# Optimization experiments

Measured on AMD Instinct MI355X. Metric: run time of the kernel, lower is better.

The kernel has to match this reference:

```python
import jax, jax.numpy as jnp
import numpy as np

N = 100000   # nodes
C = 128      # in_channels
K = 32       # n_super_nodes
B = 64       # graphs (num segments)


def setup_inputs() -> dict:
    key = jax.random.key(0)
    k_x, k_b, k_w1, k_b1, k_w2, k_b2 = jax.random.split(key, 6)
    x = jax.random.normal(k_x, (N, C), dtype=jnp.float32)
    batch = jnp.sort(jax.random.randint(k_b, (N,), 0, B))
    # assign_mlp params: Linear(C,C) -> ReLU -> Linear(C,K); stored as [in,out]
    W1 = jax.random.normal(k_w1, (C, C), dtype=jnp.float32) / np.sqrt(C)
    b1 = jax.random.normal(k_b1, (C,), dtype=jnp.float32) * 0.01
    W2 = jax.random.normal(k_w2, (C, K), dtype=jnp.float32) / np.sqrt(C)
    b2 = jax.random.normal(k_b2, (K,), dtype=jnp.float32) * 0.01
    return {"x": x, "batch": batch, "W1": W1, "b1": b1, "W2": W2, "b2": b2}


def reference(x, batch, W1, b1, W2, b2):
    # assignment logits: MLP over node features
    h = jax.nn.relu(x @ W1 + b1)          # [N, C]
    s = jax.nn.softmax(h @ W2 + b2, axis=-1)  # [N, K]
    # outer product per node, then scatter-sum by graph id
    x_expanded = x[:, None, :] * s[:, :, None]  # [N, K, C]
    out = jax.ops.segment_sum(x_expanded, batch, num_segments=B)  # [B, K, C]
    return (out, s)
```

## Files before the change

kernel.cpp:

```cpp
#include <hip/hip_runtime.h>
#include <hip/hip_bf16.h>

#define NN 100000
#define CC 128
#define KK 32
#define BB 64
#define CH 2
#define NCHUNK (NN / 32)

typedef __bf16 bf16x8 __attribute__((ext_vector_type(8)));
typedef float  f32x4  __attribute__((ext_vector_type(4)));

__device__ __forceinline__ unsigned short f2bf(float v) {
    union { __bf16 h; unsigned short s; } u;
    u.h = (__bf16)v;
    return u.s;
}
__device__ __forceinline__ float bf2f(unsigned short h) {
    union { unsigned u; float f; } a; a.u = ((unsigned)h) << 16;
    return a.f;
}
__device__ __forceinline__ void unpack_hilo(uint4 a, uint4 b,
                                            bf16x8& hi8, bf16x8& lo8) {
    union { unsigned u[4]; bf16x8 v; } H, L;
    H.u[0] = __builtin_amdgcn_perm(a.y, a.x, 0x05040100u);
    H.u[1] = __builtin_amdgcn_perm(a.w, a.z, 0x05040100u);
    H.u[2] = __builtin_amdgcn_perm(b.y, b.x, 0x05040100u);
    H.u[3] = __builtin_amdgcn_perm(b.w, b.z, 0x05040100u);
    L.u[0] = __builtin_amdgcn_perm(a.y, a.x, 0x07060302u);
    L.u[1] = __builtin_amdgcn_perm(a.w, a.z, 0x07060302u);
    L.u[2] = __builtin_amdgcn_perm(b.y, b.x, 0x07060302u);
    L.u[3] = __builtin_amdgcn_perm(b.w, b.z, 0x07060302u);
    hi8 = H.v; lo8 = L.v;
}

__device__ __forceinline__ void atomAddF(float* p, float v) {
#if defined(__gfx950__) || defined(__gfx942__) || defined(__gfx90a__)
    unsafeAtomicAdd(p, v);
#else
    atomicAdd(p, v);
#endif
}

__global__ __launch_bounds__(256) void hp_prep(const float* __restrict__ W1,
                                               const float* __restrict__ W2,
                                               unsigned short* __restrict__ w1f,
                                               unsigned short* __restrict__ w2f,
                                               float* __restrict__ out_zero) {
    const int t = blockIdx.x * 256 + threadIdx.x;
    {
        const int idx  = t;
        const int j    = idx & 7;
        const int lane = (idx >> 3) & 63;
        const int nt   = (idx >> 9) & 7;
        const int kt   = idx >> 12;
        const int k = kt * 32 + (lane >> 4) * 8 + j;
        const int n = nt * 16 + (lane & 15);
        const float w = W1[k * CC + n];
        const unsigned short h = f2bf(w);
        w1f[idx]         = h;
        w1f[16384 + idx] = f2bf(w - bf2f(h));
    }
    if (t < 4096) {
        const int idx  = t;
        const int j    = idx & 7;
        const int lane = (idx >> 3) & 63;
        const int nt   = (idx >> 9) & 1;
        const int kt   = idx >> 10;
        const int k = kt * 32 + (lane >> 4) * 8 + j;
        const int n = nt * 16 + (lane & 15);
        const float w = W2[k * KK + n];
        const unsigned short h = f2bf(w);
        w2f[idx]        = h;
        w2f[4096 + idx] = f2bf(w - bf2f(h));
    }
    const float4 z = make_float4(0.f, 0.f, 0.f, 0.f);
    for (int i = t; i < BB * KK * CC / 4; i += 16384)
        *(float4*)(out_zero + (size_t)i * 4) = z;
}

__global__ __launch_bounds__(256, 3) void hp_fused(
    const float* __restrict__ x,
    const unsigned short* __restrict__ w1f,
    const unsigned short* __restrict__ w2f,
    const float* __restrict__ b1,
    const float* __restrict__ b2,
    const int* __restrict__ batch,
    float* __restrict__ s_out,
    float* __restrict__ out)
{
    __shared__ __align__(16) char uni[16896];
    __shared__ __align__(16) unsigned short xbL[8 * 64 * 8];
    __shared__ float lgT[32][36];

    unsigned short* xa   = (unsigned short*)uni;
    unsigned int*   hs16 = (unsigned int*)uni;

    const int t    = threadIdx.x;
    const int wave = __builtin_amdgcn_readfirstlane(t >> 6);
    const int lane = t & 63;

    const int pmt   = wave & 1;
    const int chalf = wave >> 1;
    const int nrow  = (lane >> 4) * 8;

    const float b2lo = b2[lane & 15];
    const float b2hi = b2[16 + (lane & 15)];

    f32x4 pacc[4];
    #pragma unroll
    for (int i = 0; i < 4; ++i) pacc[i] = (f32x4){0.f, 0.f, 0.f, 0.f};

    int cg = __builtin_amdgcn_readfirstlane(batch[blockIdx.x * (CH * 32)]);

    auto flush = [&](int g) {
        float* op = out + (size_t)g * KK * CC;
        #pragma unroll
        for (int i = 0; i < 4; ++i) {
            const int c = (chalf * 4 + i) * 16 + (lane & 15);
            #pragma unroll
            for (int r = 0; r < 4; ++r) {
                const int k = pmt * 16 + (lane >> 4) * 4 + r;
                atomAddF(op + k * CC + c, pacc[i][r]);
            }
            pacc[i] = (f32x4){0.f, 0.f, 0.f, 0.f};
        }
    };

    #pragma unroll 1
    for (int ch = 0; ch < CH; ++ch) {
        const int chunk = blockIdx.x * CH + ch;
        if (chunk >= NCHUNK) break;
        const int base = chunk * 32;

        __syncthreads();

        #pragma unroll
        for (int mt = 0; mt < 2; ++mt) {
            const int q  = mt * 4 + wave;
            const int n  = base + mt * 16 + (lane & 15);
            const int ck = wave * 32 + (lane >> 4) * 8;
            const float4 va = *(const float4*)(x + (size_t)n * CC + ck);
            const float4 vb = *(const float4*)(x + (size_t)n * CC + ck + 4);
            const float v[8] = {va.x, va.y, va.z, va.w, vb.x, vb.y, vb.z, vb.w};
            union { unsigned short s[8]; uint4 u; } H, L;
            #pragma unroll
            for (int j = 0; j < 8; ++j) {
                H.s[j] = f2bf(v[j]);
                L.s[j] = f2bf(v[j] - bf2f(H.s[j]));
            }
            unsigned short* d0 = xa + (q * 64 + lane) * 8;
            *(uint4*)(d0)        = H.u;
            *(uint4*)(d0 + 4096) = L.u;
        }

        #pragma unroll
        for (int cc = 0; cc < 2; ++cc) {
            const int ct = wave * 2 + cc;
            const int c  = ct * 16 + (lane & 15);
            const int nb = base + nrow;
            union { unsigned short s[8]; uint4 u; } Hb;
            #pragma unroll
            for (int j = 0; j < 8; ++j)
                Hb.s[j] = f2bf(x[(size_t)(nb + j) * CC + c]);
            *(uint4*)(xbL + ((size_t)ct * 64 + lane) * 8) = Hb.u;
        }
        __syncthreads();

        f32x4 acc[2][2];
        #pragma unroll
        for (int mt = 0; mt < 2; ++mt)
            #pragma unroll
            for (int nl = 0; nl < 2; ++nl)
                acc[mt][nl] = (f32x4){0.f, 0.f, 0.f, 0.f};

        #pragma unroll
        for (int kt = 0; kt < 4; ++kt) {
            bf16x8 ah[2], al[2];
            #pragma unroll
            for (int mt = 0; mt < 2; ++mt) {
                ah[mt] = *(const bf16x8*)(xa + ((mt * 4 + kt) * 64 + lane) * 8);
                al[mt] = *(const bf16x8*)(xa + 4096 + ((mt * 4 + kt) * 64 + lane) * 8);
            }
            #pragma unroll
            for (int nl = 0; nl < 2; ++nl) {
                const int nt = 2 * wave + nl;
                const bf16x8 wh = *(const bf16x8*)(w1f + ((kt * 8 + nt) * 64 + lane) * 8);
                const bf16x8 wl = *(const bf16x8*)(w1f + 16384 + ((kt * 8 + nt) * 64 + lane) * 8);
                #pragma unroll
                for (int mt = 0; mt < 2; ++mt) {
                    acc[mt][nl] = __builtin_amdgcn_mfma_f32_16x16x32_bf16(ah[mt], wh, acc[mt][nl], 0, 0, 0);
                    acc[mt][nl] = __builtin_amdgcn_mfma_f32_16x16x32_bf16(al[mt], wh, acc[mt][nl], 0, 0, 0);
                    acc[mt][nl] = __builtin_amdgcn_mfma_f32_16x16x32_bf16(ah[mt], wl, acc[mt][nl], 0, 0, 0);
                }
            }
        }
        __syncthreads();

        #pragma unroll
        for (int nl = 0; nl < 2; ++nl) {
            const int c = (2 * wave + nl) * 16 + (lane & 15);
            const float bv = b1[c];
            #pragma unroll
            for (int mt = 0; mt < 2; ++mt)
                #pragma unroll
                for (int r = 0; r < 4; ++r) {
                    const int node = mt * 16 + (lane >> 4) * 4 + r;
                    const float h = fmaxf(acc[mt][nl][r] + bv, 0.f);
                    const unsigned short hi = f2bf(h);
                    const unsigned short lo = f2bf(h - bf2f(hi));
                    hs16[node * 132 + c] = (unsigned)hi | ((unsigned)lo << 16);
                }
        }
        __syncthreads();

        if (wave < 2) {
            const int mt2 = wave;
            f32x4 dacc[2];
            dacc[0] = (f32x4){0.f, 0.f, 0.f, 0.f};
            dacc[1] = (f32x4){0.f, 0.f, 0.f, 0.f};
            #pragma unroll
            for (int kt = 0; kt < 4; ++kt) {
                const unsigned* hp = hs16 + (mt2 * 16 + (lane & 15)) * 132
                                          + kt * 32 + (lane >> 4) * 8;
                const uint4 u0 = *(const uint4*)hp;
                const uint4 u1 = *(const uint4*)(hp + 4);
                bf16x8 ah, al;
                unpack_hilo(u0, u1, ah, al);
                #pragma unroll
                for (int nt2 = 0; nt2 < 2; ++nt2) {
                    const bf16x8 wh = *(const bf16x8*)(w2f + ((kt * 2 + nt2) * 64 + lane) * 8);
                    const bf16x8 wl = *(const bf16x8*)(w2f + 4096 + ((kt * 2 + nt2) * 64 + lane) * 8);
                    dacc[nt2] = __builtin_amdgcn_mfma_f32_16x16x32_bf16(ah, wh, dacc[nt2], 0, 0, 0);
                    dacc[nt2] = __builtin_amdgcn_mfma_f32_16x16x32_bf16(al, wh, dacc[nt2], 0, 0, 0);
                    dacc[nt2] = __builtin_amdgcn_mfma_f32_16x16x32_bf16(ah, wl, dacc[nt2], 0, 0, 0);
                }
            }
            float lg0[4], lg1[4], m[4];
            #pragma unroll
            for (int r = 0; r < 4; ++r) {
                lg0[r] = dacc[0][r] + b2lo;
                lg1[r] = dacc[1][r] + b2hi;
                m[r] = fmaxf(lg0[r], lg1[r]);
            }
            #pragma unroll
            for (int msk = 1; msk < 16; msk <<= 1)
                #pragma unroll
                for (int r = 0; r < 4; ++r)
                    m[r] = fmaxf(m[r], __shfl_xor(m[r], msk));
            float e0[4], e1[4], sm[4];
            #pragma unroll
            for (int r = 0; r < 4; ++r) {
                e0[r] = __expf(lg0[r] - m[r]);
                e1[r] = __expf(lg1[r] - m[r]);
                sm[r] = e0[r] + e1[r];
            }
            #pragma unroll
            for (int msk = 1; msk < 16; msk <<= 1)
                #pragma unroll
                for (int r = 0; r < 4; ++r)
                    sm[r] += __shfl_xor(sm[r], msk);
            #pragma unroll
            for (int r = 0; r < 4; ++r) {
                const float inv = 1.f / sm[r];
                const int node = mt2 * 16 + (lane >> 4) * 4 + r;
                lgT[node][lane & 15]        = e0[r] * inv;
                lgT[node][16 + (lane & 15)] = e1[r] * inv;
            }
        }
        __syncthreads();

        {
            const int node = lane & 31;
            const int koff = ((lane >> 5) << 4) + wave * 4;
            const float4 s4 = *(const float4*)&lgT[node][koff];
            *(float4*)(s_out + (size_t)(base + node) * KK + koff) = s4;
        }

        {
            union { unsigned short s[8]; bf16x8 v; } A;
            const int kA = pmt * 16 + (lane & 15);
            #pragma unroll
            for (int j = 0; j < 8; ++j)
                A.s[j] = f2bf(lgT[nrow + j][kA]);
            bf16x8 Bv[4];
            #pragma unroll
            for (int i = 0; i < 4; ++i)
                Bv[i] = *(const bf16x8*)(xbL + ((size_t)(chalf * 4 + i) * 64 + lane) * 8);

            const int gl0 = __builtin_amdgcn_readfirstlane(batch[base]);
            const int gh  = __builtin_amdgcn_readfirstlane(batch[base + 31]);

            if (gl0 == cg && gh == cg) {
                #pragma unroll
                for (int i = 0; i < 4; ++i)
                    pacc[i] = __builtin_amdgcn_mfma_f32_16x16x32_bf16(A.v, Bv[i], pacc[i], 0, 0, 0);
            } else {
                int bt[8];
                #pragma unroll
                for (int j = 0; j < 8; ++j) bt[j] = batch[base + nrow + j];
                while (cg < gh) {
                    union { unsigned short s[8]; bf16x8 v; } Am;
                    #pragma unroll
                    for (int j = 0; j < 8; ++j)
                        Am.s[j] = (bt[j] == cg) ? A.s[j] : (unsigned short)0;
                    #pragma unroll
                    for (int i = 0; i < 4; ++i)
                        pacc[i] = __builtin_amdgcn_mfma_f32_16x16x32_bf16(Am.v, Bv[i], pacc[i], 0, 0, 0);
                    flush(cg);
                    ++cg;
                }
                union { unsigned short s[8]; bf16x8 v; } Am;
                #pragma unroll
                for (int j = 0; j < 8; ++j)
                    Am.s[j] = (bt[j] == cg) ? A.s[j] : (unsigned short)0;
                #pragma unroll
                for (int i = 0; i < 4; ++i)
                    pacc[i] = __builtin_amdgcn_mfma_f32_16x16x32_bf16(Am.v, Bv[i], pacc[i], 0, 0, 0);
            }
        }
    }

    flush(cg);
}

extern "C" void kernel_launch(void* const* d_in, const int* in_sizes, int n_in,
                              void* d_out, int out_size, void* d_ws, size_t ws_size,
                              hipStream_t stream) {
    const float* x     = (const float*)d_in[0];
    const int*   batch = (const int*)d_in[1];
    const float* W1    = (const float*)d_in[2];
    const float* b1    = (const float*)d_in[3];
    const float* W2    = (const float*)d_in[4];
    const float* b2    = (const float*)d_in[5];

    float* out = (float*)d_out;
    float* s   = out + (size_t)BB * KK * CC;

    char* ws = (char*)d_ws;
    unsigned short* w1f = (unsigned short*)ws;
    unsigned short* w2f = (unsigned short*)(ws + 65536);

    hp_prep<<<64, 256, 0, stream>>>(W1, W2, w1f, w2f, out);
    const int nblk = (NCHUNK + CH - 1) / CH;
    hp_fused<<<nblk, 256, 0, stream>>>(x, w1f, w2f, b1, b2, batch, s, out);
}
```

Measured before the change: 137.2 us.

## Replace output atomics with per-slot partials and prefetch next chunk into registers

Each block now owns twice as many 32-node chunks. While the current chunk is being converted and computed, the block loads the next chunk's x values into registers, and the bf16 x tile buffer is double-buffered in shared memory. The per-graph float atomics on the output are replaced by plain stores into a per-graph, per-slot partial buffer. A slot is derived from segment bounds computed by binary search in the prep kernel. A new reduce kernel sums the 16 slots into the output. This trades atomic contention for an extra launch, a larger workspace to zero and reduce, and more register pressure. It also assumes no graph spans more than 16 blocks.

```diff
diff --git a/kernel.cpp b/kernel.cpp
--- a/kernel.cpp
+++ b/kernel.cpp
@@ -5,8 +5,9 @@
 #define CC 128
 #define KK 32
 #define BB 64
-#define CH 2
+#define CH 4
 #define NCHUNK (NN / 32)
+#define NSLOT 16
 
 typedef __bf16 bf16x8 __attribute__((ext_vector_type(8)));
 typedef float  f32x4  __attribute__((ext_vector_type(4)));
@@ -34,21 +35,24 @@
     hi8 = H.v; lo8 = L.v;
 }
 
-__device__ __forceinline__ void atomAddF(float* p, float v) {
-#if defined(__gfx950__) || defined(__gfx942__) || defined(__gfx90a__)
-    unsafeAtomicAdd(p, v);
-#else
-    atomicAdd(p, v);
-#endif
-}
-
-__global__ __launch_bounds__(256) void hp_prep(const float* __restrict__ W1,
+__global__ __launch_bounds__(256) void hp_prep(const int* __restrict__ batch,
+                                               const float* __restrict__ W1,
                                                const float* __restrict__ W2,
+                                               int* __restrict__ bounds,
                                                unsigned short* __restrict__ w1f,
                                                unsigned short* __restrict__ w2f,
-                                               float* __restrict__ out_zero) {
+                                               float* __restrict__ part) {
+    if (blockIdx.x == 0 && threadIdx.x <= BB) {
+        const int b = threadIdx.x;
+        int lo = 0, hi = NN;
+        while (lo < hi) {
+            const int mid = (lo + hi) >> 1;
+            if (batch[mid] < b) lo = mid + 1; else hi = mid;
+        }
+        bounds[b] = lo;
+    }
     const int t = blockIdx.x * 256 + threadIdx.x;
-    {
+    if (t < 16384) {
         const int idx  = t;
         const int j    = idx & 7;
         const int lane = (idx >> 3) & 63;
@@ -75,8 +79,8 @@
         w2f[4096 + idx] = f2bf(w - bf2f(h));
     }
     const float4 z = make_float4(0.f, 0.f, 0.f, 0.f);
-    for (int i = t; i < BB * KK * CC / 4; i += 16384)
-        *(float4*)(out_zero + (size_t)i * 4) = z;
+    for (int i = t; i < BB * NSLOT * KK * CC / 4; i += 65536)
+        *(float4*)(part + (size_t)i * 4) = z;
 }
 
 __global__ __launch_bounds__(256, 3) void hp_fused(
@@ -86,11 +90,12 @@
     const float* __restrict__ b1,
     const float* __restrict__ b2,
     const int* __restrict__ batch,
+    const int* __restrict__ bounds,
     float* __restrict__ s_out,
-    float* __restrict__ out)
+    float* __restrict__ part)
 {
     __shared__ __align__(16) char uni[16896];
-    __shared__ __align__(16) unsigned short xbL[8 * 64 * 8];
+    __shared__ __align__(16) unsigned short xbL[2][8 * 64 * 8];
     __shared__ float lgT[32][36];
 
     unsigned short* xa   = (unsigned short*)uni;
@@ -104,6 +109,8 @@
     const int chalf = wave >> 1;
     const int nrow  = (lane >> 4) * 8;
 
+    const float bv_epi0 = b1[(2 * wave + 0) * 16 + (lane & 15)];
+    const float bv_epi1 = b1[(2 * wave + 1) * 16 + (lane & 15)];
     const float b2lo = b2[lane & 15];
     const float b2hi = b2[16 + (lane & 15)];
 
@@ -114,18 +121,40 @@
     int cg = __builtin_amdgcn_readfirstlane(batch[blockIdx.x * (CH * 32)]);
 
     auto flush = [&](int g) {
-        float* op = out + (size_t)g * KK * CC;
+        const int slot = blockIdx.x - (bounds[g] >> 7);
+        float* op = part + ((size_t)g * NSLOT + slot) * (KK * CC);
         #pragma unroll
         for (int i = 0; i < 4; ++i) {
             const int c = (chalf * 4 + i) * 16 + (lane & 15);
             #pragma unroll
             for (int r = 0; r < 4; ++r) {
                 const int k = pmt * 16 + (lane >> 4) * 4 + r;
-                atomAddF(op + k * CC + c, pacc[i][r]);
+                op[k * CC + c] = pacc[i][r];
             }
             pacc[i] = (f32x4){0.f, 0.f, 0.f, 0.f};
         }
     };
+
+    float4 pva0, pvb0, pva1, pvb1;
+    float  pxb0[8], pxb1[8];
+    {
+        const int base0 = blockIdx.x * (CH * 32);
+        const int n0 = base0 + (lane & 15);
+        const int n1 = base0 + 16 + (lane & 15);
+        const int ck = wave * 32 + (lane >> 4) * 8;
+        pva0 = *(const float4*)(x + (size_t)n0 * CC + ck);
+        pvb0 = *(const float4*)(x + (size_t)n0 * CC + ck + 4);
+        pva1 = *(const float4*)(x + (size_t)n1 * CC + ck);
+        pvb1 = *(const float4*)(x + (size_t)n1 * CC + ck + 4);
+        const int c0 = (wave * 2 + 0) * 16 + (lane & 15);
+        const int c1 = (wave * 2 + 1) * 16 + (lane & 15);
+        const int nr = base0 + nrow;
+        #pragma unroll
+        for (int j = 0; j < 8; ++j) {
+            pxb0[j] = x[(size_t)(nr + j) * CC + c0];
+            pxb1[j] = x[(size_t)(nr + j) * CC + c1];
+        }
+    }
 
     #pragma unroll 1
     for (int ch = 0; ch < CH; ++ch) {
@@ -133,37 +162,53 @@
         if (chunk >= NCHUNK) break;
         const int base = chunk * 32;
 
-        __syncthreads();
-
-        #pragma unroll
-        for (int mt = 0; mt < 2; ++mt) {
-            const int q  = mt * 4 + wave;
-            const int n  = base + mt * 16 + (lane & 15);
+        {
+            const float v0[8] = {pva0.x, pva0.y, pva0.z, pva0.w,
+                                 pvb0.x, pvb0.y, pvb0.z, pvb0.w};
+            const float v1[8] = {pva1.x, pva1.y, pva1.z, pva1.w,
+                                 pvb1.x, pvb1.y, pvb1.z, pvb1.w};
+            union { unsigned short s[8]; uint4 u; } H0, L0, H1, L1;
+            #pragma unroll
+            for (int j = 0; j < 8; ++j) {
+                H0.s[j] = f2bf(v0[j]); L0.s[j] = f2bf(v0[j] - bf2f(H0.s[j]));
+                H1.s[j] = f2bf(v1[j]); L1.s[j] = f2bf(v1[j] - bf2f(H1.s[j]));
+            }
+            unsigned short* d0 = xa + ((0 * 4 + wave) * 64 + lane) * 8;
+            unsigned short* d1 = xa + ((1 * 4 + wave) * 64 + lane) * 8;
+            *(uint4*)(d0)        = H0.u;
+            *(uint4*)(d0 + 4096) = L0.u;
+            *(uint4*)(d1)        = H1.u;
+            *(uint4*)(d1 + 4096) = L1.u;
+        }
+
+        {
+            union { unsigned short s[8]; uint4 u; } Hb0, Hb1;
+            #pragma unroll
+            for (int j = 0; j < 8; ++j) {
+                Hb0.s[j] = f2bf(pxb0[j]);
+                Hb1.s[j] = f2bf(pxb1[j]);
+            }
+            *(uint4*)(&xbL[ch & 1][((wave * 2 + 0) * 64 + lane) * 8]) = Hb0.u;
+            *(uint4*)(&xbL[ch & 1][((wave * 2 + 1) * 64 + lane) * 8]) = Hb1.u;
+        }
+
+        if (ch + 1 < CH && chunk + 1 < NCHUNK) {
+            const int nb = base + 32;
+            const int n0 = nb + (lane & 15);
+            const int n1 = nb + 16 + (lane & 15);
             const int ck = wave * 32 + (lane >> 4) * 8;
-            const float4 va = *(const float4*)(x + (size_t)n * CC + ck);
-            const float4 vb = *(const float4*)(x + (size_t)n * CC + ck + 4);
-            const float v[8] = {va.x, va.y, va.z, va.w, vb.x, vb.y, vb.z, vb.w};
-            union { unsigned short s[8]; uint4 u; } H, L;
+            pva0 = *(const float4*)(x + (size_t)n0 * CC + ck);
+            pvb0 = *(const float4*)(x + (size_t)n0 * CC + ck + 4);
+            pva1 = *(const float4*)(x + (size_t)n1 * CC + ck);
+            pvb1 = *(const float4*)(x + (size_t)n1 * CC + ck + 4);
+            const int c0 = (wave * 2 + 0) * 16 + (lane & 15);
+            const int c1 = (wave * 2 + 1) * 16 + (lane & 15);
+            const int nr = nb + nrow;
             #pragma unroll
             for (int j = 0; j < 8; ++j) {
-                H.s[j] = f2bf(v[j]);
-                L.s[j] = f2bf(v[j] - bf2f(H.s[j]));
-            }
-            unsigned short* d0 = xa + (q * 64 + lane) * 8;
-            *(uint4*)(d0)        = H.u;
-            *(uint4*)(d0 + 4096) = L.u;
-        }
-
-        #pragma unroll
-        for (int cc = 0; cc < 2; ++cc) {
-            const int ct = wave * 2 + cc;
-            const int c  = ct * 16 + (lane & 15);
-            const int nb = base + nrow;
-            union { unsigned short s[8]; uint4 u; } Hb;
-            #pragma unroll
-            for (int j = 0; j < 8; ++j)
-                Hb.s[j] = f2bf(x[(size_t)(nb + j) * CC + c]);
-            *(uint4*)(xbL + ((size_t)ct * 64 + lane) * 8) = Hb.u;
+                pxb0[j] = x[(size_t)(nr + j) * CC + c0];
+                pxb1[j] = x[(size_t)(nr + j) * CC + c1];
+            }
         }
         __syncthreads();
 
@@ -199,8 +244,8 @@
 
         #pragma unroll
         for (int nl = 0; nl < 2; ++nl) {
+            const float bv = nl ? bv_epi1 : bv_epi0;
             const int c = (2 * wave + nl) * 16 + (lane & 15);
-            const float bv = b1[c];
             #pragma unroll
             for (int mt = 0; mt < 2; ++mt)
                 #pragma unroll
@@ -286,7 +331,7 @@
             bf16x8 Bv[4];
             #pragma unroll
             for (int i = 0; i < 4; ++i)
-                Bv[i] = *(const bf16x8*)(xbL + ((size_t)(chalf * 4 + i) * 64 + lane) * 8);
+                Bv[i] = *(const bf16x8*)(&xbL[ch & 1][((chalf * 4 + i) * 64 + lane) * 8]);
 
             const int gl0 = __builtin_amdgcn_readfirstlane(batch[base]);
             const int gh  = __builtin_amdgcn_readfirstlane(batch[base + 31]);
@@ -324,6 +369,23 @@
     flush(cg);
 }
 
+__global__ __launch_bounds__(256) void hp_reduce(const float* __restrict__ part,
+                                                 float* __restrict__ out) {
+    const int i = (blockIdx.x * 256 + threadIdx.x) * 4;
+    if (i < BB * KK * CC) {
+        const int b = i >> 12;
+        const int j = i & 4095;
+        const float* pp = part + (size_t)b * NSLOT * 4096 + j;
+        float4 r = make_float4(0.f, 0.f, 0.f, 0.f);
+        #pragma unroll 4
+        for (int q = 0; q < NSLOT; ++q) {
+            const float4 v = *(const float4*)(pp + (size_t)q * 4096);
+            r.x += v.x; r.y += v.y; r.z += v.z; r.w += v.w;
+        }
+        *(float4*)(out + i) = r;
+    }
+}
+
 extern "C" void kernel_launch(void* const* d_in, const int* in_sizes, int n_in,
                               void* d_out, int out_size, void* d_ws, size_t ws_size,
                               hipStream_t stream) {
@@ -338,10 +400,13 @@
     float* s   = out + (size_t)BB * KK * CC;
 
     char* ws = (char*)d_ws;
-    unsigned short* w1f = (unsigned short*)ws;
-    unsigned short* w2f = (unsigned short*)(ws + 65536);
-
-    hp_prep<<<64, 256, 0, stream>>>(W1, W2, w1f, w2f, out);
+    int*            bounds = (int*)ws;
+    unsigned short* w1f    = (unsigned short*)(ws + 1024);
+    unsigned short* w2f    = (unsigned short*)(ws + 66560);
+    float*          part   = (float*)(ws + 82944);
+
+    hp_prep<<<256, 256, 0, stream>>>(batch, W1, W2, bounds, w1f, w2f, part);
     const int nblk = (NCHUNK + CH - 1) / CH;
-    hp_fused<<<nblk, 256, 0, stream>>>(x, w1f, w2f, b1, b2, batch, s, out);
-}
+    hp_fused<<<nblk, 256, 0, stream>>>(x, w1f, w2f, b1, b2, batch, bounds, s, part);
+    hp_reduce<<<BB * KK * CC / (256 * 4), 256, 0, stream>>>(part, out);
+}
```

Measured after the change: 173.9 us. +26.7%, slower.

## Replace global atomics with per-block partial slots plus separate reduction kernel

Applied to the files above, without the earlier changes.

Each block now writes its per-graph partial sums to a dedicated slot computed from binary-searched segment bounds, and a new reduce kernel sums 16 slots per graph. This removes contended float atomics on the output. It also doubles chunks per block, double-buffers the xbL tile so one barrier per chunk can be dropped, hoists the b1 bias loads, and moves the s store after the MFMA. In exchange it adds an extra kernel launch, zeroes a much larger partial buffer, and relies on each graph spanning at most 16 blocks (slot = block - bounds>>7).

```diff
diff --git a/kernel.cpp b/kernel.cpp
--- a/kernel.cpp
+++ b/kernel.cpp
@@ -5,8 +5,9 @@
 #define CC 128
 #define KK 32
 #define BB 64
-#define CH 2
+#define CH 4
 #define NCHUNK (NN / 32)
+#define NSLOT 16
 
 typedef __bf16 bf16x8 __attribute__((ext_vector_type(8)));
 typedef float  f32x4  __attribute__((ext_vector_type(4)));
@@ -34,21 +35,24 @@
     hi8 = H.v; lo8 = L.v;
 }
 
-__device__ __forceinline__ void atomAddF(float* p, float v) {
-#if defined(__gfx950__) || defined(__gfx942__) || defined(__gfx90a__)
-    unsafeAtomicAdd(p, v);
-#else
-    atomicAdd(p, v);
-#endif
-}
-
-__global__ __launch_bounds__(256) void hp_prep(const float* __restrict__ W1,
+__global__ __launch_bounds__(256) void hp_prep(const int* __restrict__ batch,
+                                               const float* __restrict__ W1,
                                                const float* __restrict__ W2,
+                                               int* __restrict__ bounds,
                                                unsigned short* __restrict__ w1f,
                                                unsigned short* __restrict__ w2f,
-                                               float* __restrict__ out_zero) {
+                                               float* __restrict__ part) {
+    if (blockIdx.x == 0 && threadIdx.x <= BB) {
+        const int b = threadIdx.x;
+        int lo = 0, hi = NN;
+        while (lo < hi) {
+            const int mid = (lo + hi) >> 1;
+            if (batch[mid] < b) lo = mid + 1; else hi = mid;
+        }
+        bounds[b] = lo;
+    }
     const int t = blockIdx.x * 256 + threadIdx.x;
-    {
+    if (t < 16384) {
         const int idx  = t;
         const int j    = idx & 7;
         const int lane = (idx >> 3) & 63;
@@ -75,8 +79,8 @@
         w2f[4096 + idx] = f2bf(w - bf2f(h));
     }
     const float4 z = make_float4(0.f, 0.f, 0.f, 0.f);
-    for (int i = t; i < BB * KK * CC / 4; i += 16384)
-        *(float4*)(out_zero + (size_t)i * 4) = z;
+    for (int i = t; i < BB * NSLOT * KK * CC / 4; i += 65536)
+        *(float4*)(part + (size_t)i * 4) = z;
 }
 
 __global__ __launch_bounds__(256, 3) void hp_fused(
@@ -86,11 +90,12 @@
     const float* __restrict__ b1,
     const float* __restrict__ b2,
     const int* __restrict__ batch,
+    const int* __restrict__ bounds,
     float* __restrict__ s_out,
-    float* __restrict__ out)
+    float* __restrict__ part)
 {
     __shared__ __align__(16) char uni[16896];
-    __shared__ __align__(16) unsigned short xbL[8 * 64 * 8];
+    __shared__ __align__(16) unsigned short xbL[2][8 * 64 * 8];
     __shared__ float lgT[32][36];
 
     unsigned short* xa   = (unsigned short*)uni;
@@ -104,6 +109,8 @@
     const int chalf = wave >> 1;
     const int nrow  = (lane >> 4) * 8;
 
+    const float bv_epi0 = b1[(2 * wave + 0) * 16 + (lane & 15)];
+    const float bv_epi1 = b1[(2 * wave + 1) * 16 + (lane & 15)];
     const float b2lo = b2[lane & 15];
     const float b2hi = b2[16 + (lane & 15)];
 
@@ -114,14 +121,15 @@
     int cg = __builtin_amdgcn_readfirstlane(batch[blockIdx.x * (CH * 32)]);
 
     auto flush = [&](int g) {
-        float* op = out + (size_t)g * KK * CC;
+        const int slot = blockIdx.x - (bounds[g] >> 7);
+        float* op = part + ((size_t)g * NSLOT + slot) * (KK * CC);
         #pragma unroll
         for (int i = 0; i < 4; ++i) {
             const int c = (chalf * 4 + i) * 16 + (lane & 15);
             #pragma unroll
             for (int r = 0; r < 4; ++r) {
                 const int k = pmt * 16 + (lane >> 4) * 4 + r;
-                atomAddF(op + k * CC + c, pacc[i][r]);
+                op[k * CC + c] = pacc[i][r];
             }
             pacc[i] = (f32x4){0.f, 0.f, 0.f, 0.f};
         }
@@ -132,8 +140,6 @@
         const int chunk = blockIdx.x * CH + ch;
         if (chunk >= NCHUNK) break;
         const int base = chunk * 32;
-
-        __syncthreads();
 
         #pragma unroll
         for (int mt = 0; mt < 2; ++mt) {
@@ -163,7 +169,7 @@
             #pragma unroll
             for (int j = 0; j < 8; ++j)
                 Hb.s[j] = f2bf(x[(size_t)(nb + j) * CC + c]);
-            *(uint4*)(xbL + ((size_t)ct * 64 + lane) * 8) = Hb.u;
+            *(uint4*)(&xbL[ch & 1][((size_t)ct * 64 + lane) * 8]) = Hb.u;
         }
         __syncthreads();
 
@@ -199,8 +205,8 @@
 
         #pragma unroll
         for (int nl = 0; nl < 2; ++nl) {
+            const float bv = nl ? bv_epi1 : bv_epi0;
             const int c = (2 * wave + nl) * 16 + (lane & 15);
-            const float bv = b1[c];
             #pragma unroll
             for (int mt = 0; mt < 2; ++mt)
                 #pragma unroll
@@ -271,13 +277,6 @@
         __syncthreads();
 
         {
-            const int node = lane & 31;
-            const int koff = ((lane >> 5) << 4) + wave * 4;
-            const float4 s4 = *(const float4*)&lgT[node][koff];
-            *(float4*)(s_out + (size_t)(base + node) * KK + koff) = s4;
-        }
-
-        {
             union { unsigned short s[8]; bf16x8 v; } A;
             const int kA = pmt * 16 + (lane & 15);
             #pragma unroll
@@ -286,7 +285,7 @@
             bf16x8 Bv[4];
             #pragma unroll
             for (int i = 0; i < 4; ++i)
-                Bv[i] = *(const bf16x8*)(xbL + ((size_t)(chalf * 4 + i) * 64 + lane) * 8);
+                Bv[i] = *(const bf16x8*)(&xbL[ch & 1][((size_t)(chalf * 4 + i) * 64 + lane) * 8]);
 
             const int gl0 = __builtin_amdgcn_readfirstlane(batch[base]);
             const int gh  = __builtin_amdgcn_readfirstlane(batch[base + 31]);
@@ -319,9 +318,33 @@
                     pacc[i] = __builtin_amdgcn_mfma_f32_16x16x32_bf16(Am.v, Bv[i], pacc[i], 0, 0, 0);
             }
         }
+
+        {
+            const int node = lane & 31;
+            const int koff = ((lane >> 5) << 4) + wave * 4;
+            const float4 s4 = *(const float4*)&lgT[node][koff];
+            *(float4*)(s_out + (size_t)(base + node) * KK + koff) = s4;
+        }
     }
 
     flush(cg);
+}
+
+__global__ __launch_bounds__(256) void hp_reduce(const float* __restrict__ part,
+                                                 float* __restrict__ out) {
+    const int i = (blockIdx.x * 256 + threadIdx.x) * 4;
+    if (i < BB * KK * CC) {
+        const int b = i >> 12;
+        const int j = i & 4095;
+        const float* pp = part + (size_t)b * NSLOT * 4096 + j;
+        float4 r = make_float4(0.f, 0.f, 0.f, 0.f);
+        #pragma unroll 4
+        for (int q = 0; q < NSLOT; ++q) {
+            const float4 v = *(const float4*)(pp + (size_t)q * 4096);
+            r.x += v.x; r.y += v.y; r.z += v.z; r.w += v.w;
+        }
+        *(float4*)(out + i) = r;
+    }
 }
 
 extern "C" void kernel_launch(void* const* d_in, const int* in_sizes, int n_in,
@@ -338,10 +361,13 @@
     float* s   = out + (size_t)BB * KK * CC;
 
     char* ws = (char*)d_ws;
-    unsigned short* w1f = (unsigned short*)ws;
-    unsigned short* w2f = (unsigned short*)(ws + 65536);
-
-    hp_prep<<<64, 256, 0, stream>>>(W1, W2, w1f, w2f, out);
+    int*            bounds = (int*)ws;
+    unsigned short* w1f    = (unsigned short*)(ws + 1024);
+    unsigned short* w2f    = (unsigned short*)(ws + 66560);
+    float*          part   = (float*)(ws + 82944);
+
+    hp_prep<<<256, 256, 0, stream>>>(batch, W1, W2, bounds, w1f, w2f, part);
     const int nblk = (NCHUNK + CH - 1) / CH;
-    hp_fused<<<nblk, 256, 0, stream>>>(x, w1f, w2f, b1, b2, batch, s, out);
-}
+    hp_fused<<<nblk, 256, 0, stream>>>(x, w1f, w2f, b1, b2, batch, bounds, s, part);
+    hp_reduce<<<BB * KK * CC / (256 * 4), 256, 0, stream>>>(part, out);
+}
```

Result: slower. 161.4 us (+17.6%).
